# Kernel optimization log

Measured on AMD Instinct MI355X. Metric: run time of the kernel, lower is better.

Reference implementation:

```python
import jax, jax.numpy as jnp
import numpy as np

NUM_HEADS = 16  # CLIP ViT-L num_attention_heads


def setup_inputs() -> dict:
    key = jax.random.key(0)
    ks = jax.random.split(key, 11)
    B, T, E = 16, 577, 1024
    d = {
        "hidden_states": jax.random.normal(ks[0], (B, T, E), jnp.float32),
        # token 'size' from prior merging steps; sizes are >= 1 in practice
        "size": jax.random.uniform(ks[1], (B, T), jnp.float32) + 1.0,
        "wq": jax.random.normal(ks[2], (E, E), jnp.float32) * (E ** -0.5),
        "bq": jax.random.normal(ks[3], (E,), jnp.float32) * 0.02,
        "wk": jax.random.normal(ks[4], (E, E), jnp.float32) * (E ** -0.5),
        "bk": jax.random.normal(ks[5], (E,), jnp.float32) * 0.02,
        "wv": jax.random.normal(ks[6], (E, E), jnp.float32) * (E ** -0.5),
        "bv": jax.random.normal(ks[7], (E,), jnp.float32) * 0.02,
        "wo": jax.random.normal(ks[8], (E, E), jnp.float32) * (E ** -0.5),
        "bo": jax.random.normal(ks[9], (E,), jnp.float32) * 0.02,
    }
    return d


def reference(hidden_states, size, wq, bq, wk, bk, wv, bv, wo, bo):
    B, T, E = hidden_states.shape
    H = NUM_HEADS
    D = E // H
    scale = D ** -0.5

    # torch nn.Linear: y = x @ W.T + b
    q = (hidden_states @ wq.T + bq) * scale
    k = hidden_states @ wk.T + bk
    v = hidden_states @ wv.T + bv

    def split_heads(x):  # [B,T,E] -> [B,H,T,D]
        return x.reshape(B, T, H, D).transpose(0, 2, 1, 3)

    qh, kh, vh = split_heads(q), split_heads(k), split_heads(v)

    # raw logits (before size bias), [B,H,T,T]
    attn_logits = jnp.einsum("bhtd,bhsd->bhts", qh, kh)

    # att_score: mean over the flattened bsz*num_heads dim, on raw logits
    att_score = attn_logits.mean(axis=(0, 1))  # [T,T]

    # additive log-size bias over keys
    attn_logits = attn_logits + jnp.log(size)[:, None, None, :]

    probs = jax.nn.softmax(attn_logits, axis=-1)  # dropout p=0 / eval
    out = jnp.einsum("bhts,bhsd->bhtd", probs, vh)
    out = out.transpose(0, 2, 1, 3).reshape(B, T, E)
    attn_output = out @ wo.T + bo

    # mean over heads of key states: [B,T,D]
    mean_keys = kh.mean(axis=1)

    return attn_output, mean_keys, att_score
```

## Files before the change

kernel.cpp:

```cpp
#include <hip/hip_runtime.h>
#include <hip/hip_bf16.h>
#include <math.h>

typedef __attribute__((ext_vector_type(8))) short s16x8;
typedef __attribute__((ext_vector_type(4))) short s16x4;
typedef __attribute__((ext_vector_type(4))) float f32x4;
typedef __attribute__((ext_vector_type(8))) __bf16 bf16x8;

#define MFMA16(a, b, c) __builtin_amdgcn_mfma_f32_16x16x32_bf16( \
    __builtin_bit_cast(bf16x8, (a)), __builtin_bit_cast(bf16x8, (b)), (c), 0, 0, 0)

__device__ __forceinline__ short f2b(float f) {
    union { float f; unsigned u; } x; x.f = f;
    unsigned u = x.u;
    unsigned r = (u + 0x7FFFu + ((u >> 16) & 1u)) >> 16;
    return (short)r;
}
__device__ __forceinline__ float b2f(short b) {
    union { unsigned u; float f; } x;
    x.u = ((unsigned)(unsigned short)b) << 16;
    return x.f;
}

__device__ __forceinline__ void gload16(const void* g, void* l) {
    __builtin_amdgcn_global_load_lds(
        (const __attribute__((address_space(1))) unsigned int*)g,
        (__attribute__((address_space(3))) unsigned int*)l, 16, 0, 0);
}

__global__ void k_f32_to_bf16(const float* __restrict__ in, short* __restrict__ out, long n) {
    long i = ((long)blockIdx.x * blockDim.x + threadIdx.x) * 4;
    long stride = (long)gridDim.x * blockDim.x * 4;
    for (; i < n; i += stride) {
        float4 v = *(const float4*)(in + i);
        s16x4 o = { f2b(v.x), f2b(v.y), f2b(v.z), f2b(v.w) };
        *(s16x4*)(out + i) = o;
    }
}

__global__ void k_wconv4(const float* __restrict__ w0, const float* __restrict__ w1,
                         const float* __restrict__ w2, const float* __restrict__ w3,
                         short* __restrict__ out, long n) {
    int wsel = blockIdx.y;
    const float* src = (wsel == 0) ? w0 : (wsel == 1) ? w1 : (wsel == 2) ? w2 : w3;
    short* dst = out + (long)wsel * n;
    long i = ((long)blockIdx.x * blockDim.x + threadIdx.x) * 4;
    if (i >= n) return;
    float4 v = *(const float4*)(src + i);
    s16x4 o = { f2b(v.x), f2b(v.y), f2b(v.z), f2b(v.w) };
    *(s16x4*)(dst + i) = o;
}

__global__ void k_sizepad(const float* __restrict__ size, float* __restrict__ out,
                          int B, int T, int SP) {
    int i = blockIdx.x * blockDim.x + threadIdx.x;
    if (i >= B * SP) return;
    int b = i / SP, s = i % SP;
    out[i] = (s < T) ? size[b * T + s] : 0.f;
}

__device__ __forceinline__ void stage_half(const short* __restrict__ src, int ldk,
                                           int row0, int maxrow, int k0,
                                           short* lds, int tid) {
    #pragma unroll
    for (int j = 0; j < 2; ++j) {
        int ch = tid + j * 512;
        int r = ch >> 3;
        int cby = ((ch & 7) * 16) ^ ((r & 7) << 4);
        int gr = row0 + r; gr = gr < maxrow ? gr : maxrow - 1;
        gload16((const char*)(src + (long)gr * ldk + k0) + cby,
                (char*)lds + ch * 16);
    }
}

__device__ __forceinline__ s16x8 lds_frag(const short* half, int r, int ks, int lg) {
    int cby = ((ks << 6) + (lg << 4)) ^ ((r & 7) << 4);
    return *(const s16x8*)((const char*)half + r * 128 + cby);
}

template<bool ROUTE>
__global__ __launch_bounds__(512, 2) void k_gemm8(
    const short* __restrict__ A, const short* __restrict__ Bw,
    const float* __restrict__ bb0, const float* __restrict__ bb1, const float* __restrict__ bb2,
    short* __restrict__ o0, short* __restrict__ o1, short* __restrict__ o2,
    float* __restrict__ Cf, int M, int N, int K, int Ntiles, float alpha0) {

    __shared__ short AS[2][2][128 * 64];
    __shared__ short BS[2][2][128 * 64];

    int nwg = gridDim.x, orig = blockIdx.x;
    int qq = nwg >> 3, rr = nwg & 7;
    int xcd = orig & 7, pos = orig >> 3;
    int wg = (xcd < rr ? xcd * (qq + 1) : rr * (qq + 1) + (xcd - rr) * qq) + pos;
    int bx = wg % Ntiles, by = wg / Ntiles;
    int row0 = by * 256, col0 = bx * 256;

    int tid = threadIdx.x;
    int lane = tid & 63, wave = tid >> 6;
    int wm = wave >> 2, wn = wave & 3;
    int lr = lane & 15, lg = lane >> 4;
    int bh = wn >> 1, brb = (wn & 1) * 64;

    f32x4 acc[8][4];
    #pragma unroll
    for (int i = 0; i < 8; i++)
        #pragma unroll
        for (int j = 0; j < 4; j++)
            #pragma unroll
            for (int q = 0; q < 4; q++) acc[i][j][q] = 0.f;

    int nt = K >> 6;
    stage_half(A,  K, row0,       M, 0, AS[0][0], tid);
    stage_half(A,  K, row0 + 128, M, 0, AS[0][1], tid);
    stage_half(Bw, K, col0,       N, 0, BS[0][0], tid);
    stage_half(Bw, K, col0 + 128, N, 0, BS[0][1], tid);

    for (int t = 0; t < nt; ++t) {
        int cur = t & 1;
        asm volatile("s_waitcnt vmcnt(0)" ::: "memory");
        __builtin_amdgcn_s_barrier();
        if (t + 1 < nt) {
            int k1 = (t + 1) << 6;
            stage_half(A,  K, row0,       M, k1, AS[cur ^ 1][0], tid);
            stage_half(A,  K, row0 + 128, M, k1, AS[cur ^ 1][1], tid);
            stage_half(Bw, K, col0,       N, k1, BS[cur ^ 1][0], tid);
            stage_half(Bw, K, col0 + 128, N, k1, BS[cur ^ 1][1], tid);
        }
        const short* Ah = AS[cur][wm];
        const short* Bh = BS[cur][bh];
        s16x8 bf[4][2];
        #pragma unroll
        for (int nf = 0; nf < 4; ++nf)
            #pragma unroll
            for (int ks = 0; ks < 2; ++ks)
                bf[nf][ks] = lds_frag(Bh, brb + nf * 16 + lr, ks, lg);
        #pragma unroll
        for (int p = 0; p < 4; ++p) {
            s16x8 af[2][2];
            #pragma unroll
            for (int i = 0; i < 2; ++i)
                #pragma unroll
                for (int ks = 0; ks < 2; ++ks)
                    af[i][ks] = lds_frag(Ah, (2 * p + i) * 16 + lr, ks, lg);
            __builtin_amdgcn_s_setprio(1);
            #pragma unroll
            for (int i = 0; i < 2; ++i)
                #pragma unroll
                for (int nf = 0; nf < 4; ++nf)
                    #pragma unroll
                    for (int ks = 0; ks < 2; ++ks)
                        acc[2 * p + i][nf] = MFMA16(af[i][ks], bf[nf][ks], acc[2 * p + i][nf]);
            __builtin_amdgcn_s_setprio(0);
        }
    }

    int wrow = row0 + wm * 128;
    #pragma unroll
    for (int mf = 0; mf < 8; ++mf) {
        int grow = wrow + mf * 16 + lg * 4;
        #pragma unroll
        for (int nf = 0; nf < 4; ++nf) {
            int gc = col0 + wn * 64 + nf * 16 + lr;
            if (gc >= N) continue;
            if (ROUTE) {
                int which = gc >> 10, lc = gc & 1023;
                float bias = (which == 0 ? bb0 : which == 1 ? bb1 : bb2)[lc];
                float alpha = (which == 0) ? alpha0 : 1.0f;
                short* op = (which == 0 ? o0 : which == 1 ? o1 : o2);
                #pragma unroll
                for (int q = 0; q < 4; ++q) {
                    int r2 = grow + q;
                    if (r2 < M) op[(long)r2 * 1024 + lc] = f2b((acc[mf][nf][q] + bias) * alpha);
                }
            } else {
                float bias = bb0[gc];
                #pragma unroll
                for (int q = 0; q < 4; ++q) {
                    int r2 = grow + q;
                    if (r2 < M) Cf[(long)r2 * N + gc] = acc[mf][nf][q] + bias;
                }
            }
        }
    }
}

__device__ __forceinline__ void gemm_core(
    const short* __restrict__ Ab, const short* __restrict__ Bb,
    float* __restrict__ Cf, int M, int N, int K, int ldc, int row0, int col0) {
    __shared__ short As[128 * 64];
    __shared__ short Bs[128 * 64];
    int tid = threadIdx.x;
    int lane = tid & 63, wave = tid >> 6;
    int wr = wave >> 1, wc = wave & 1;
    int lr = lane & 15, lg = lane >> 4;
    f32x4 acc[4][4];
    #pragma unroll
    for (int i = 0; i < 4; i++)
        #pragma unroll
        for (int j = 0; j < 4; j++)
            #pragma unroll
            for (int q = 0; q < 4; q++) acc[i][j][q] = 0.f;

    for (int k0 = 0; k0 < K; k0 += 64) {
        __syncthreads();
        #pragma unroll
        for (int i = 0; i < 4; ++i) {
            int cw = i * 256 + wave * 64;
            int c = cw + lane;
            int r = c >> 3;
            int cby = ((c & 7) * 16) ^ ((r & 7) << 4);
            int ra = row0 + r; ra = ra < M ? ra : M - 1;
            gload16((const char*)(Ab + (long)ra * K + k0) + cby, &As[cw * 8]);
            int rb = col0 + r; rb = rb < N ? rb : N - 1;
            gload16((const char*)(Bb + (long)rb * K + k0) + cby, &Bs[cw * 8]);
        }
        __syncthreads();
        #pragma unroll
        for (int ks = 0; ks < 2; ++ks) {
            s16x8 af[4], bfr[4];
            #pragma unroll
            for (int i = 0; i < 4; ++i) {
                int r = wr * 64 + i * 16 + lr;
                af[i] = *(const s16x8*)((const char*)As + r * 128 +
                        (((ks << 6) + (lg << 4)) ^ ((r & 7) << 4)));
            }
            #pragma unroll
            for (int j = 0; j < 4; ++j) {
                int r = wc * 64 + j * 16 + lr;
                bfr[j] = *(const s16x8*)((const char*)Bs + r * 128 +
                         (((ks << 6) + (lg << 4)) ^ ((r & 7) << 4)));
            }
            #pragma unroll
            for (int i = 0; i < 4; ++i)
                #pragma unroll
                for (int j = 0; j < 4; ++j)
                    acc[i][j] = MFMA16(af[i], bfr[j], acc[i][j]);
        }
    }
    #pragma unroll
    for (int i = 0; i < 4; i++) {
        int rbase = row0 + wr * 64 + i * 16 + lg * 4;
        #pragma unroll
        for (int j = 0; j < 4; j++) {
            int c = col0 + wc * 64 + j * 16 + lr;
            if (c >= N) continue;
            #pragma unroll
            for (int q = 0; q < 4; q++) {
                int r = rbase + q;
                if (r >= M) continue;
                Cf[(long)r * ldc + c] = acc[i][j][q];
            }
        }
    }
}

__global__ __launch_bounds__(256) void k_att(
    const short* __restrict__ q, const short* __restrict__ k,
    float* __restrict__ attp, int T, int E) {
    int z = blockIdx.z;
    gemm_core(q + (long)z * T * E, k + (long)z * T * E,
              attp + (long)z * T * T, T, T, E, T,
              blockIdx.y * 128, blockIdx.x * 128);
}

__global__ void k_mean_keys8(const short* __restrict__ Kb, float* __restrict__ out, int BT) {
    int i = blockIdx.x * blockDim.x + threadIdx.x;
    if (i >= BT * 8) return;
    int bt = i >> 3, d0 = (i & 7) * 8;
    const short* p = Kb + (long)bt * 1024 + d0;
    float s[8] = {0.f, 0.f, 0.f, 0.f, 0.f, 0.f, 0.f, 0.f};
    #pragma unroll
    for (int h = 0; h < 16; ++h) {
        s16x8 v = *(const s16x8*)(p + h * 64);
        #pragma unroll
        for (int j = 0; j < 8; ++j) s[j] += b2f(v[j]);
    }
    float4 o0 = {s[0] * 0.0625f, s[1] * 0.0625f, s[2] * 0.0625f, s[3] * 0.0625f};
    float4 o1 = {s[4] * 0.0625f, s[5] * 0.0625f, s[6] * 0.0625f, s[7] * 0.0625f};
    *(float4*)(out + (long)bt * 64 + d0) = o0;
    *(float4*)(out + (long)bt * 64 + d0 + 4) = o1;
}

__global__ void k_att_reduce(const float* __restrict__ part, float* __restrict__ out,
                             int n, int nb, long stride) {
    int i = blockIdx.x * blockDim.x + threadIdx.x;
    if (i >= n) return;
    float s = 0.f;
    for (int b = 0; b < nb; ++b) s += part[(long)b * stride + i];
    out[i] = s * 0.002707606174062286f;
}

__global__ __launch_bounds__(256) void k_vtrans(const short* __restrict__ v, short* __restrict__ vt,
                                                int B, int T, int H, int TP) {
    int b = blockIdx.z, h = blockIdx.y, t0 = blockIdx.x * 64;
    __shared__ short Vs[64][68];
    int tid = threadIdx.x;
    for (int c = tid; c < 512; c += 256) {
        int r = c >> 3, m = c & 7;
        s16x8 val = {0,0,0,0,0,0,0,0};
        if (t0 + r < T) val = *(const s16x8*)(v + ((long)(b * T + t0 + r)) * (H * 64) + h * 64 + m * 8);
        *(s16x8*)&Vs[r][m * 8] = val;
    }
    __syncthreads();
    for (int c = tid; c < 512; c += 256) {
        int d = c >> 3, mw = c & 7;
        s16x8 o;
        #pragma unroll
        for (int j = 0; j < 8; j++) o[j] = Vs[mw * 8 + j][d];
        *(s16x8*)(vt + ((long)((b * H + h) * 64 + d)) * TP + t0 + mw * 8) = o;
    }
}

__global__ __launch_bounds__(256) void k_flash(
    const short* __restrict__ Q, const short* __restrict__ Kb, const short* __restrict__ VT,
    const float* __restrict__ szp, short* __restrict__ Ctx,
    int B, int T, int E, int H, int SP, int TP, int NTQ) {
    int nwg = gridDim.x;
    int cpx = nwg >> 3;
    int wg = (blockIdx.x & 7) * cpx + (blockIdx.x >> 3);
    int tq = wg % NTQ, h = (wg / NTQ) % H, b = wg / (NTQ * H);
    int t0 = tq * 128;

    __shared__ short Ks[64][68];
    __shared__ short Vt[64][68];
    __shared__ short Ps[4][32][68];
    __shared__ float Ls[64];
    int tid = threadIdx.x, wid = tid >> 6, lane = tid & 63;
    int lr = lane & 15, lg = lane >> 4;

    s16x8 aqf[2][2];
    #pragma unroll
    for (int i = 0; i < 2; ++i) {
        int t = t0 + wid * 32 + i * 16 + lr; t = t < T ? t : T - 1;
        #pragma unroll
        for (int ks = 0; ks < 2; ++ks)
            aqf[i][ks] = *(const s16x8*)(Q + ((long)b * T + t) * E + h * 64 + ks * 32 + lg * 8);
    }

    const short* kb  = Kb + (long)b * T * E + h * 64;
    const short* vtb = VT + ((long)(b * H + h)) * 64 * TP;

    int c0 = tid, c1 = tid + 256;
    int r0 = c0 >> 3, m0 = c0 & 7, r1 = c1 >> 3, m1 = c1 & 7;
    s16x8 kreg0, kreg1, vreg0, vreg1;
    float lreg = 0.f;

    {
        int s = r0; s = s < T ? s : T - 1;
        kreg0 = *(const s16x8*)(kb + (long)s * E + m0 * 8);
        s = r1; s = s < T ? s : T - 1;
        kreg1 = *(const s16x8*)(kb + (long)s * E + m1 * 8);
        vreg0 = *(const s16x8*)(vtb + (long)r0 * TP + 0 + m0 * 8);
        vreg1 = *(const s16x8*)(vtb + (long)r1 * TP + 0 + m1 * 8);
        if (tid < 64) lreg = szp[b * SP + 0 + tid];
    }

    float mreg[2][4], lsum[2][4];
    f32x4 o[2][4];
    #pragma unroll
    for (int i = 0; i < 2; i++)
        #pragma unroll
        for (int q = 0; q < 4; q++) { mreg[i][q] = -INFINITY; lsum[i][q] = 0.f; }
    #pragma unroll
    for (int i = 0; i < 2; i++)
        #pragma unroll
        for (int jd = 0; jd < 4; jd++)
            #pragma unroll
            for (int q = 0; q < 4; q++) o[i][jd][q] = 0.f;

    for (int s0 = 0; s0 < T; s0 += 64) {
        *(s16x8*)&Ks[r0][m0 * 8] = kreg0;
        *(s16x8*)&Ks[r1][m1 * 8] = kreg1;
        *(s16x8*)&Vt[r0][m0 * 8] = vreg0;
        *(s16x8*)&Vt[r1][m1 * 8] = vreg1;
        if (tid < 64) Ls[tid] = lreg;
        __syncthreads();

        if (s0 + 64 < T) {
            int sn = s0 + 64;
            int s = sn + r0; s = s < T ? s : T - 1;
            kreg0 = *(const s16x8*)(kb + (long)s * E + m0 * 8);
            s = sn + r1; s = s < T ? s : T - 1;
            kreg1 = *(const s16x8*)(kb + (long)s * E + m1 * 8);
            vreg0 = *(const s16x8*)(vtb + (long)r0 * TP + sn + m0 * 8);
            vreg1 = *(const s16x8*)(vtb + (long)r1 * TP + sn + m1 * 8);
            if (tid < 64) lreg = szp[b * SP + sn + tid];
        }

        float szv[4];
        #pragma unroll
        for (int j = 0; j < 4; j++) szv[j] = Ls[j * 16 + lr];

        s16x8 kf[2][4];
        #pragma unroll
        for (int ks = 0; ks < 2; ++ks)
            #pragma unroll
            for (int j = 0; j < 4; ++j)
                kf[ks][j] = *(const s16x8*)&Ks[j * 16 + lr][ks * 32 + lg * 8];

        #pragma unroll
        for (int i = 0; i < 2; ++i) {
            f32x4 sf[4];
            #pragma unroll
            for (int j = 0; j < 4; j++)
                #pragma unroll
                for (int q = 0; q < 4; q++) sf[j][q] = 0.f;
            __builtin_amdgcn_s_setprio(1);
            #pragma unroll
            for (int ks = 0; ks < 2; ++ks)
                #pragma unroll
                for (int j = 0; j < 4; j++) sf[j] = MFMA16(aqf[i][ks], kf[ks][j], sf[j]);
            __builtin_amdgcn_s_setprio(0);

            float tmax[4];
            #pragma unroll
            for (int q = 0; q < 4; q++)
                tmax[q] = fmaxf(fmaxf(sf[0][q], sf[1][q]), fmaxf(sf[2][q], sf[3][q]));
            int ok = 1;
            #pragma unroll
            for (int q = 0; q < 4; q++) ok &= (tmax[q] <= mreg[i][q] + 11.0f) ? 1 : 0;
            if (!__all(ok)) {
                #pragma unroll
                for (int q = 0; q < 4; q++) {
                    #pragma unroll
                    for (int msk = 1; msk < 16; msk <<= 1)
                        tmax[q] = fmaxf(tmax[q], __shfl_xor(tmax[q], msk));
                    float mn = fmaxf(mreg[i][q], tmax[q]);
                    float al = exp2f(mreg[i][q] - mn);
                    mreg[i][q] = mn;
                    lsum[i][q] *= al;
                    #pragma unroll
                    for (int jd = 0; jd < 4; jd++) o[i][jd][q] *= al;
                }
            }
            float rs[4] = {0.f, 0.f, 0.f, 0.f};
            #pragma unroll
            for (int j = 0; j < 4; j++) {
                float szj = szv[j];
                #pragma unroll
                for (int q = 0; q < 4; q++) {
                    float p = exp2f(sf[j][q] - mreg[i][q]) * szj;
                    sf[j][q] = p;
                    rs[q] += p;
                }
            }
            #pragma unroll
            for (int q = 0; q < 4; q++) lsum[i][q] += rs[q];

            #pragma unroll
            for (int j = 0; j < 4; j++)
                #pragma unroll
                for (int q = 0; q < 4; q++)
                    Ps[wid][i * 16 + lg * 4 + q][j * 16 + lr] = f2b(sf[j][q]);

            __builtin_amdgcn_s_setprio(1);
            #pragma unroll
            for (int ks = 0; ks < 2; ++ks) {
                s16x8 ap = *(const s16x8*)&Ps[wid][i * 16 + lr][ks * 32 + lg * 8];
                #pragma unroll
                for (int jd = 0; jd < 4; jd++) {
                    s16x8 bv = *(const s16x8*)&Vt[jd * 16 + lr][ks * 32 + lg * 8];
                    o[i][jd] = MFMA16(ap, bv, o[i][jd]);
                }
            }
            __builtin_amdgcn_s_setprio(0);
        }
        __syncthreads();
    }

    short* cb = Ctx + ((long)b * T + t0) * E + h * 64;
    #pragma unroll
    for (int i = 0; i < 2; i++)
        #pragma unroll
        for (int q = 0; q < 4; q++) {
            float s = lsum[i][q];
            s += __shfl_xor(s, 1); s += __shfl_xor(s, 2);
            s += __shfl_xor(s, 4); s += __shfl_xor(s, 8);
            int t = wid * 32 + i * 16 + lg * 4 + q;
            if (t0 + t >= T) continue;
            float inv = 1.f / s;
            #pragma unroll
            for (int jd = 0; jd < 4; jd++)
                cb[(long)t * E + jd * 16 + lr] = f2b(o[i][jd][q] * inv);
        }
}

extern "C" void kernel_launch(void* const* d_in, const int* in_sizes, int n_in,
                              void* d_out, int out_size, void* d_ws, size_t ws_size,
                              hipStream_t stream) {
    (void)in_sizes; (void)n_in; (void)out_size; (void)ws_size;
    const int B = 16, T = 577, E = 1024, H = 16;
    const int SP = 640, TP = 640;
    const float* hs   = (const float*)d_in[0];
    const float* size = (const float*)d_in[1];
    const float* wq   = (const float*)d_in[2];
    const float* bq   = (const float*)d_in[3];
    const float* wk   = (const float*)d_in[4];
    const float* bk   = (const float*)d_in[5];
    const float* wv   = (const float*)d_in[6];
    const float* bv   = (const float*)d_in[7];
    const float* wo   = (const float*)d_in[8];
    const float* bo   = (const float*)d_in[9];

    float* out_attn = (float*)d_out;
    float* out_mk   = out_attn + (long)B * T * E;
    float* out_as   = out_mk + (long)B * T * 64;

    long nBTE = (long)B * T * E;
    long nEE  = (long)E * E;
    char* ws = (char*)d_ws;
    short* hs_b  = (short*)ws; ws += nBTE * 2;
    short* wq_b  = (short*)ws; ws += nEE * 2;
    short* wk_b  = (short*)ws; ws += nEE * 2;
    short* wv_b  = (short*)ws; ws += nEE * 2;
    short* wo_b  = (short*)ws; ws += nEE * 2;
    short* q_b   = (short*)ws; ws += nBTE * 2;
    short* k_b   = (short*)ws; ws += nBTE * 2;
    short* v_b   = (short*)ws; ws += nBTE * 2;
    short* ctx_b = (short*)ws; ws += nBTE * 2;
    float* szpad = (float*)ws; ws += (long)B * SP * 4;
    float* att_p = (float*)ws; ws += (long)B * T * T * 4;
    short* vt = (short*)att_p;

    k_f32_to_bf16<<<2048, 256, 0, stream>>>(hs, hs_b, nBTE);
    {
        dim3 gw((nEE / 4 + 255) / 256, 4);
        k_wconv4<<<gw, 256, 0, stream>>>(wq, wk, wv, wo, wq_b, nEE);
    }
    k_sizepad<<<(B * SP + 255) / 256, 256, 0, stream>>>(size, szpad, B, T, SP);

    int M = B * T;
    {
        int Mtiles = (M + 255) / 256, Ntiles = 3072 / 256;
        k_gemm8<true><<<Mtiles * Ntiles, 512, 0, stream>>>(
            hs_b, wq_b, bq, bk, bv, q_b, k_b, v_b, nullptr, M, 3072, E, Ntiles,
            0.18033688011112042f);
    }

    dim3 g_att((T + 127) / 128, (T + 127) / 128, B);
    k_att<<<g_att, dim3(256), 0, stream>>>(q_b, k_b, att_p, T, E);
    k_att_reduce<<<((T * T) + 255) / 256, 256, 0, stream>>>(att_p, out_as, T * T, B, (long)T * T);

    dim3 g_vt((T + 63) / 64, H, B);
    k_vtrans<<<g_vt, dim3(256), 0, stream>>>(v_b, vt, B, T, H, TP);

    k_mean_keys8<<<((B * T * 8) + 255) / 256, 256, 0, stream>>>(k_b, out_mk, B * T);

    const int NTQ = (T + 127) / 128;
    int nfl = NTQ * H * B;
    k_flash<<<nfl, dim3(256), 0, stream>>>(q_b, k_b, vt, szpad, ctx_b, B, T, E, H, SP, TP, NTQ);

    {
        int Mtiles = (M + 255) / 256, Ntiles = 1024 / 256;
        k_gemm8<false><<<Mtiles * Ntiles, 512, 0, stream>>>(
            ctx_b, wo_b, bo, nullptr, nullptr, nullptr, nullptr, nullptr,
            out_attn, M, 1024, E, Ntiles, 1.0f);
    }
}
```

Baseline: 304.4 us.

## Replace 256x256 double-buffered GEMM with simpler 128x128 single-buffered kernel

Swaps the 512-thread, 256x256-tile, double-buffered projection GEMM for a 256-thread, 128x128-tile kernel with a single LDS buffer and two barriers per K step. Smaller tiles give more workgroups and less LDS per block, which may raise occupancy and help tail balance on the 9232-row problem. In exchange it loses the overlap of global loads with MFMA work and halves data reuse per tile, so global/LDS traffic per FLOP rises.

Result: faster. 296.3 us (-2.7%).

```diff
diff --git a/kernel.cpp b/kernel.cpp
--- a/kernel.cpp
+++ b/kernel.cpp
@@ -59,108 +59,79 @@
     out[i] = (s < T) ? size[b * T + s] : 0.f;
 }
 
-__device__ __forceinline__ void stage_half(const short* __restrict__ src, int ldk,
-                                           int row0, int maxrow, int k0,
-                                           short* lds, int tid) {
-    #pragma unroll
-    for (int j = 0; j < 2; ++j) {
-        int ch = tid + j * 512;
-        int r = ch >> 3;
-        int cby = ((ch & 7) * 16) ^ ((r & 7) << 4);
-        int gr = row0 + r; gr = gr < maxrow ? gr : maxrow - 1;
-        gload16((const char*)(src + (long)gr * ldk + k0) + cby,
-                (char*)lds + ch * 16);
-    }
-}
-
-__device__ __forceinline__ s16x8 lds_frag(const short* half, int r, int ks, int lg) {
-    int cby = ((ks << 6) + (lg << 4)) ^ ((r & 7) << 4);
-    return *(const s16x8*)((const char*)half + r * 128 + cby);
-}
-
 template<bool ROUTE>
-__global__ __launch_bounds__(512, 2) void k_gemm8(
+__global__ __launch_bounds__(256) void k_gemm4(
     const short* __restrict__ A, const short* __restrict__ Bw,
     const float* __restrict__ bb0, const float* __restrict__ bb1, const float* __restrict__ bb2,
     short* __restrict__ o0, short* __restrict__ o1, short* __restrict__ o2,
     float* __restrict__ Cf, int M, int N, int K, int Ntiles, float alpha0) {
 
-    __shared__ short AS[2][2][128 * 64];
-    __shared__ short BS[2][2][128 * 64];
+    __shared__ short As[128 * 64];
+    __shared__ short Bs[128 * 64];
 
     int nwg = gridDim.x, orig = blockIdx.x;
     int qq = nwg >> 3, rr = nwg & 7;
     int xcd = orig & 7, pos = orig >> 3;
     int wg = (xcd < rr ? xcd * (qq + 1) : rr * (qq + 1) + (xcd - rr) * qq) + pos;
     int bx = wg % Ntiles, by = wg / Ntiles;
-    int row0 = by * 256, col0 = bx * 256;
+    int row0 = by * 128, col0 = bx * 128;
 
     int tid = threadIdx.x;
     int lane = tid & 63, wave = tid >> 6;
-    int wm = wave >> 2, wn = wave & 3;
+    int wr = wave >> 1, wc = wave & 1;
     int lr = lane & 15, lg = lane >> 4;
-    int bh = wn >> 1, brb = (wn & 1) * 64;
-
-    f32x4 acc[8][4];
-    #pragma unroll
-    for (int i = 0; i < 8; i++)
+
+    f32x4 acc[4][4];
+    #pragma unroll
+    for (int i = 0; i < 4; i++)
         #pragma unroll
         for (int j = 0; j < 4; j++)
             #pragma unroll
             for (int q = 0; q < 4; q++) acc[i][j][q] = 0.f;
 
-    int nt = K >> 6;
-    stage_half(A,  K, row0,       M, 0, AS[0][0], tid);
-    stage_half(A,  K, row0 + 128, M, 0, AS[0][1], tid);
-    stage_half(Bw, K, col0,       N, 0, BS[0][0], tid);
-    stage_half(Bw, K, col0 + 128, N, 0, BS[0][1], tid);
-
-    for (int t = 0; t < nt; ++t) {
-        int cur = t & 1;
-        asm volatile("s_waitcnt vmcnt(0)" ::: "memory");
-        __builtin_amdgcn_s_barrier();
-        if (t + 1 < nt) {
-            int k1 = (t + 1) << 6;
-            stage_half(A,  K, row0,       M, k1, AS[cur ^ 1][0], tid);
-            stage_half(A,  K, row0 + 128, M, k1, AS[cur ^ 1][1], tid);
-            stage_half(Bw, K, col0,       N, k1, BS[cur ^ 1][0], tid);
-            stage_half(Bw, K, col0 + 128, N, k1, BS[cur ^ 1][1], tid);
-        }
-        const short* Ah = AS[cur][wm];
-        const short* Bh = BS[cur][bh];
-        s16x8 bf[4][2];
-        #pragma unroll
-        for (int nf = 0; nf < 4; ++nf)
-            #pragma unroll
-            for (int ks = 0; ks < 2; ++ks)
-                bf[nf][ks] = lds_frag(Bh, brb + nf * 16 + lr, ks, lg);
-        #pragma unroll
-        for (int p = 0; p < 4; ++p) {
-            s16x8 af[2][2];
-            #pragma unroll
-            for (int i = 0; i < 2; ++i)
-                #pragma unroll
-                for (int ks = 0; ks < 2; ++ks)
-                    af[i][ks] = lds_frag(Ah, (2 * p + i) * 16 + lr, ks, lg);
-            __builtin_amdgcn_s_setprio(1);
-            #pragma unroll
-            for (int i = 0; i < 2; ++i)
-                #pragma unroll
-                for (int nf = 0; nf < 4; ++nf)
-                    #pragma unroll
-                    for (int ks = 0; ks < 2; ++ks)
-                        acc[2 * p + i][nf] = MFMA16(af[i][ks], bf[nf][ks], acc[2 * p + i][nf]);
-            __builtin_amdgcn_s_setprio(0);
-        }
-    }
-
-    int wrow = row0 + wm * 128;
-    #pragma unroll
-    for (int mf = 0; mf < 8; ++mf) {
-        int grow = wrow + mf * 16 + lg * 4;
-        #pragma unroll
-        for (int nf = 0; nf < 4; ++nf) {
-            int gc = col0 + wn * 64 + nf * 16 + lr;
+    for (int k0 = 0; k0 < K; k0 += 64) {
+        __syncthreads();
+        #pragma unroll
+        for (int i = 0; i < 4; ++i) {
+            int cw = i * 256 + wave * 64;
+            int c = cw + lane;
+            int r = c >> 3;
+            int cby = ((c & 7) * 16) ^ ((r & 7) << 4);
+            int ra = row0 + r; ra = ra < M ? ra : M - 1;
+            gload16((const char*)(A + (long)ra * K + k0) + cby, &As[cw * 8]);
+            int rb = col0 + r; rb = rb < N ? rb : N - 1;
+            gload16((const char*)(Bw + (long)rb * K + k0) + cby, &Bs[cw * 8]);
+        }
+        __syncthreads();
+        #pragma unroll
+        for (int ks = 0; ks < 2; ++ks) {
+            s16x8 af[4], bfr[4];
+            #pragma unroll
+            for (int i = 0; i < 4; ++i) {
+                int r = wr * 64 + i * 16 + lr;
+                af[i] = *(const s16x8*)((const char*)As + r * 128 +
+                        (((ks << 6) + (lg << 4)) ^ ((r & 7) << 4)));
+            }
+            #pragma unroll
+            for (int j = 0; j < 4; ++j) {
+                int r = wc * 64 + j * 16 + lr;
+                bfr[j] = *(const s16x8*)((const char*)Bs + r * 128 +
+                         (((ks << 6) + (lg << 4)) ^ ((r & 7) << 4)));
+            }
+            #pragma unroll
+            for (int i = 0; i < 4; ++i)
+                #pragma unroll
+                for (int j = 0; j < 4; ++j)
+                    acc[i][j] = MFMA16(af[i], bfr[j], acc[i][j]);
+        }
+    }
+
+    #pragma unroll
+    for (int i = 0; i < 4; i++) {
+        int grow0 = row0 + wr * 64 + i * 16 + lg * 4;
+        #pragma unroll
+        for (int j = 0; j < 4; j++) {
+            int gc = col0 + wc * 64 + j * 16 + lr;
             if (gc >= N) continue;
             if (ROUTE) {
                 int which = gc >> 10, lc = gc & 1023;
@@ -169,15 +140,15 @@
                 short* op = (which == 0 ? o0 : which == 1 ? o1 : o2);
                 #pragma unroll
                 for (int q = 0; q < 4; ++q) {
-                    int r2 = grow + q;
-                    if (r2 < M) op[(long)r2 * 1024 + lc] = f2b((acc[mf][nf][q] + bias) * alpha);
+                    int r2 = grow0 + q;
+                    if (r2 < M) op[(long)r2 * 1024 + lc] = f2b((acc[i][j][q] + bias) * alpha);
                 }
             } else {
                 float bias = bb0[gc];
                 #pragma unroll
                 for (int q = 0; q < 4; ++q) {
-                    int r2 = grow + q;
-                    if (r2 < M) Cf[(long)r2 * N + gc] = acc[mf][nf][q] + bias;
+                    int r2 = grow0 + q;
+                    if (r2 < M) Cf[(long)r2 * N + gc] = acc[i][j][q] + bias;
                 }
             }
         }
@@ -531,8 +502,8 @@
 
     int M = B * T;
     {
-        int Mtiles = (M + 255) / 256, Ntiles = 3072 / 256;
-        k_gemm8<true><<<Mtiles * Ntiles, 512, 0, stream>>>(
+        int Mtiles = (M + 127) / 128, Ntiles = 3072 / 128;
+        k_gemm4<true><<<Mtiles * Ntiles, 256, 0, stream>>>(
             hs_b, wq_b, bq, bk, bv, q_b, k_b, v_b, nullptr, M, 3072, E, Ntiles,
             0.18033688011112042f);
     }
@@ -551,8 +522,8 @@
     k_flash<<<nfl, dim3(256), 0, stream>>>(q_b, k_b, vt, szpad, ctx_b, B, T, E, H, SP, TP, NTQ);
 
     {
-        int Mtiles = (M + 255) / 256, Ntiles = 1024 / 256;
-        k_gemm8<false><<<Mtiles * Ntiles, 512, 0, stream>>>(
+        int Mtiles = (M + 127) / 128, Ntiles = 1024 / 128;
+        k_gemm4<false><<<Mtiles * Ntiles, 256, 0, stream>>>(
             ctx_b, wo_b, bo, nullptr, nullptr, nullptr, nullptr, nullptr,
             out_attn, M, 1024, E, Ntiles, 1.0f);
     }
```
